# Optimization experiments

Measured on AMD Instinct MI355X. Metric: run time of the kernel, lower is better.

The kernel has to match this reference:

```python
import jax, jax.numpy as jnp
import numpy as np

B, L, D = 4, 2048, 1024
N_HEADS = 16
D_KV = D // N_HEADS  # 64
TEMPERATURE = D_KV ** 0.5  # 8.0 (note: applied even though heads are never split)


def setup_inputs() -> dict:
    key = jax.random.key(0)
    ks = jax.random.split(key, 7)
    s = 1.0 / np.sqrt(D)
    return {
        "Q": jax.random.normal(ks[0], (B, L, D), jnp.float32),
        "K": jax.random.normal(ks[1], (B, L, D), jnp.float32),
        "V": jax.random.normal(ks[2], (B, L, D), jnp.float32),
        # nn.Linear weights, shape [out, in]; y = x @ W.T
        "W_Q": jax.random.normal(ks[3], (D, D), jnp.float32) * s,
        "W_K": jax.random.normal(ks[4], (D, D), jnp.float32) * s,
        "W_V": jax.random.normal(ks[5], (D, D), jnp.float32) * s,
        "W_O": jax.random.normal(ks[6], (D, D), jnp.float32) * s,
        "masked": 0,
    }


def reference(Q, K, V, W_Q, W_K, W_V, W_O, masked):
    # projections (no bias)
    q = jnp.einsum("bld,ed->ble", Q, W_Q)
    k = jnp.einsum("bld,ed->ble", K, W_K)
    v = jnp.einsum("bld,ed->ble", V, W_V)
    # NOTE: original module never splits heads; scores contract over full d_model
    scores = jnp.einsum("bqe,bke->bqk", q, k) / TEMPERATURE  # [B, L, L]
    if masked:
        # faithful (buggy) original: fill where tril is True
        tril = jnp.tril(jnp.ones((L, L), dtype=bool))
        scores = jnp.where(tril[None], -jnp.inf, scores)
    attn_weights = jax.nn.softmax(scores, axis=-1)
    # dropout(0.1) disabled (eval mode)
    x = jnp.einsum("bqk,bke->bqe", attn_weights, v)
    out = jnp.einsum("ble,de->bld", x, W_O)
    return (out, attn_weights)
```

## Files before the change

kernel.cpp:

```cpp
#include <hip/hip_runtime.h>
#include <math.h>


static constexpr int B_ = 4;
static constexpr int L_ = 2048;
static constexpr int D_ = 1024;

#define BM 128
#define BN 128
#define BKK 64

typedef _Float16 f16x8 __attribute__((ext_vector_type(8)));
typedef float    f32x4 __attribute__((ext_vector_type(4)));
typedef short    s16x8 __attribute__((ext_vector_type(8)));
typedef unsigned short u16x4 __attribute__((ext_vector_type(4)));

typedef __attribute__((address_space(1))) const unsigned int GU32;
typedef __attribute__((address_space(3))) unsigned int LU32;

__device__ __forceinline__ void gload_lds16(const void* g, void* l) {
    __builtin_amdgcn_global_load_lds((GU32*)g, (LU32*)l, 16, 0, 0);
}

__device__ __forceinline__ short f2h_bits(float x) {
    union { _Float16 h; short s; } u;
    u.h = (_Float16)x;
    return u.s;
}

__device__ __forceinline__ s16x8 cvt8h(float4 a, float4 b) {
    union { _Float16 h[8]; s16x8 s; } u;
    u.h[0] = (_Float16)a.x; u.h[1] = (_Float16)a.y;
    u.h[2] = (_Float16)a.z; u.h[3] = (_Float16)a.w;
    u.h[4] = (_Float16)b.x; u.h[5] = (_Float16)b.y;
    u.h[6] = (_Float16)b.z; u.h[7] = (_Float16)b.w;
    return u.s;
}

__device__ __forceinline__ void compute_step(
    const short* __restrict__ As, const short* __restrict__ Bs,
    int wr, int wc, int lr, int lk, f32x4 (&acc)[4][4])
{
#pragma unroll
    for (int kk = 0; kk < 2; ++kk) {
        const int slotk = kk * 4 + lk;
        f16x8 a[4], b[4];
#pragma unroll
        for (int m = 0; m < 4; ++m) {
            const int r = wr * 64 + m * 16 + lr;
            a[m] = *(const f16x8*)&As[r * 64 + ((slotk ^ (r & 7)) << 3)];
        }
#pragma unroll
        for (int n = 0; n < 4; ++n) {
            const int c = wc * 64 + n * 16 + lr;
            b[n] = *(const f16x8*)&Bs[c * 64 + ((slotk ^ (c & 7)) << 3)];
        }
#pragma unroll
        for (int m = 0; m < 4; ++m)
#pragma unroll
            for (int n = 0; n < 4; ++n)
                acc[m][n] = __builtin_amdgcn_mfma_f32_16x16x32_f16(a[m], b[n], acc[m][n], 0, 0, 0);
    }
}

__global__ __launch_bounds__(256) void proj_qkv(
    const short* __restrict__ qf, const short* __restrict__ kf, const short* __restrict__ vf,
    const short* __restrict__ wq, const short* __restrict__ wk, const short* __restrict__ wv,
    short* __restrict__ qh, short* __restrict__ kh, short* __restrict__ vT)
{
    __shared__ short As[BM * BKK];
    __shared__ short Bs[BN * BKK];

    const int t    = threadIdx.x;
    const int wid  = t >> 6;
    const int lane = t & 63;
    const int bz   = blockIdx.z;

    const short* A16 = (bz == 0) ? qf : (bz == 1) ? kf : vf;
    const short* Bt  = (bz == 0) ? wq : (bz == 1) ? wk : wv;

    const int gx = gridDim.x, gy = gridDim.y;
    const int wg = blockIdx.y * gx + blockIdx.x;
    const int bm = (wg % gy) * BM;
    const int bn = (wg / gy) * BN;

    const int wr = wid >> 1, wc = wid & 1;
    const int lr = lane & 15, lk = lane >> 4;
    const int srow = t >> 3, sslot = t & 7;
    const int K = D_;

    f32x4 acc[4][4];
#pragma unroll
    for (int m = 0; m < 4; ++m)
#pragma unroll
        for (int n = 0; n < 4; ++n) acc[m][n] = (f32x4)0.f;

    for (int k0 = 0; k0 < K; k0 += BKK) {
        __syncthreads();
#pragma unroll
        for (int i = 0; i < 4; ++i) {
            const int rb = i * 32 + srow;
            const short* g = Bt + (long)(bn + rb) * K + k0 + ((sslot ^ (rb & 7)) << 3);
            gload_lds16(g, &Bs[i * 2048 + wid * 512]);
        }
#pragma unroll
        for (int i = 0; i < 4; ++i) {
            const int ra = i * 32 + srow;
            const short* g = A16 + (long)(bm + ra) * K + k0 + ((sslot ^ (ra & 7)) << 3);
            gload_lds16(g, &As[i * 2048 + wid * 512]);
        }
        __syncthreads();
        compute_step(As, Bs, wr, wc, lr, lk, acc);
    }

    const int N = D_;
    if (bz < 2) {
        short* C = (bz == 0) ? qh : kh;
#pragma unroll
        for (int m = 0; m < 4; ++m) {
            const int r0 = bm + wr * 64 + m * 16 + lk * 4;
#pragma unroll
            for (int n = 0; n < 4; ++n) {
                const int c = bn + wc * 64 + n * 16 + lr;
#pragma unroll
                for (int g = 0; g < 4; ++g)
                    C[(long)(r0 + g) * N + c] = f2h_bits(acc[m][n][g]);
            }
        }
    } else {
#pragma unroll
        for (int m = 0; m < 4; ++m) {
            const int rg = bm + wr * 64 + m * 16 + lk * 4;
            const long rb = (long)(rg >> 11) * ((long)N * L_) + (rg & (L_ - 1));
#pragma unroll
            for (int n = 0; n < 4; ++n) {
                const int c = bn + wc * 64 + n * 16 + lr;
                u16x4 v;
#pragma unroll
                for (int g = 0; g < 4; ++g) v[g] = (unsigned short)f2h_bits(acc[m][n][g]);
                *(u16x4*)&vT[rb + (long)c * L_] = v;
            }
        }
    }
}

template<int OMODE>
__global__ __launch_bounds__(256) void hgemm(
    const short* __restrict__ A16p, const short* __restrict__ Btp, void* __restrict__ Cp_,
    int M, int N, int K, long sA, long sB, long sC,
    float scale, int useMask, const int* __restrict__ mflag)
{
    __shared__ short As[BM * BKK];
    __shared__ short Bs[BN * BKK];

    const int t    = threadIdx.x;
    const int wid  = t >> 6;
    const int lane = t & 63;
    const int bz   = blockIdx.z;

    const int gx = gridDim.x, gy = gridDim.y;
    const int wg = blockIdx.y * gx + blockIdx.x;
    const int bm = (wg % gy) * BM;
    const int bn = (wg / gy) * BN;

    const short* Bt  = Btp + (long)bz * sB;
    const short* A16 = A16p + (long)bz * sA;

    const int wr = wid >> 1, wc = wid & 1;
    const int lr = lane & 15, lk = lane >> 4;
    const int srow = t >> 3, sslot = t & 7;

    f32x4 acc[4][4];
#pragma unroll
    for (int m = 0; m < 4; ++m)
#pragma unroll
        for (int n = 0; n < 4; ++n) acc[m][n] = (f32x4)0.f;

    for (int k0 = 0; k0 < K; k0 += BKK) {
        __syncthreads();
#pragma unroll
        for (int i = 0; i < 4; ++i) {
            const int rb = i * 32 + srow;
            const short* g = Bt + (long)(bn + rb) * K + k0 + ((sslot ^ (rb & 7)) << 3);
            gload_lds16(g, &Bs[i * 2048 + wid * 512]);
        }
#pragma unroll
        for (int i = 0; i < 4; ++i) {
            const int ra = i * 32 + srow;
            const short* g = A16 + (long)(bm + ra) * K + k0 + ((sslot ^ (ra & 7)) << 3);
            gload_lds16(g, &As[i * 2048 + wid * 512]);
        }
        __syncthreads();
        compute_step(As, Bs, wr, wc, lr, lk, acc);
    }

    if constexpr (OMODE == 2) {
        float* C = (float*)Cp_ + (long)bz * sC;
        const bool msk = useMask && (mflag[0] != 0);
#pragma unroll
        for (int m = 0; m < 4; ++m) {
            const int r0 = bm + wr * 64 + m * 16 + lk * 4;
#pragma unroll
            for (int n = 0; n < 4; ++n) {
                const int c = bn + wc * 64 + n * 16 + lr;
#pragma unroll
                for (int g = 0; g < 4; ++g) {
                    float v = acc[m][n][g] * scale;
                    if (msk && c <= r0 + g) v = -INFINITY;
                    C[(long)(r0 + g) * N + c] = v;
                }
            }
        }
    } else {
        short* C = (short*)Cp_ + (long)bz * sC;
#pragma unroll
        for (int m = 0; m < 4; ++m) {
            const int r0 = bm + wr * 64 + m * 16 + lk * 4;
#pragma unroll
            for (int n = 0; n < 4; ++n) {
                const int c = bn + wc * 64 + n * 16 + lr;
#pragma unroll
                for (int g = 0; g < 4; ++g)
                    C[(long)(r0 + g) * N + c] = f2h_bits(acc[m][n][g]);
            }
        }
    }
}

__global__ __launch_bounds__(256) void cvt_w4_k(
    const float* __restrict__ W_Q, const float* __restrict__ W_K,
    const float* __restrict__ W_V, const float* __restrict__ W_O,
    short* __restrict__ dst)
{
    const int w = blockIdx.y;
    const float* src = (w == 0) ? W_Q : (w == 1) ? W_K : (w == 2) ? W_V : W_O;
    short* out = dst + (size_t)w * D_ * D_;
    const int i = blockIdx.x * 256 + threadIdx.x;
    float4 a = ((const float4*)src)[2 * i];
    float4 b = ((const float4*)src)[2 * i + 1];
    *(s16x8*)&out[i * 8] = cvt8h(a, b);
}

__global__ __launch_bounds__(256) void cvt_qkv_k(
    const float* __restrict__ Q, const float* __restrict__ K,
    const float* __restrict__ V, short* __restrict__ dst)
{
    const int w = blockIdx.y;
    const float* src = (w == 0) ? Q : (w == 1) ? K : V;
    short* out = dst + (size_t)w * B_ * L_ * D_;
    const int i = blockIdx.x * 256 + threadIdx.x;
    float4 a = ((const float4*)src)[2 * i];
    float4 b = ((const float4*)src)[2 * i + 1];
    *(s16x8*)&out[i * 8] = cvt8h(a, b);
}

__global__ __launch_bounds__(256) void softmax_rows_k(
    float* __restrict__ S, short* __restrict__ S16)
{
    const long row = blockIdx.x;
    float* p = S + row * (long)L_;
    short* p16 = S16 + row * (long)L_;
    const int tid = threadIdx.x;

    float4 v0 = ((const float4*)p)[tid];
    float4 v1 = ((const float4*)p)[tid + 256];

    float m = fmaxf(fmaxf(fmaxf(v0.x, v0.y), fmaxf(v0.z, v0.w)),
                    fmaxf(fmaxf(v1.x, v1.y), fmaxf(v1.z, v1.w)));
#pragma unroll
    for (int o = 32; o > 0; o >>= 1) m = fmaxf(m, __shfl_xor(m, o, 64));

    __shared__ float wmax[4], wsum[4];
    if ((tid & 63) == 0) wmax[tid >> 6] = m;
    __syncthreads();
    m = fmaxf(fmaxf(wmax[0], wmax[1]), fmaxf(wmax[2], wmax[3]));

    v0.x = expf(v0.x - m); v0.y = expf(v0.y - m);
    v0.z = expf(v0.z - m); v0.w = expf(v0.w - m);
    v1.x = expf(v1.x - m); v1.y = expf(v1.y - m);
    v1.z = expf(v1.z - m); v1.w = expf(v1.w - m);

    float s = v0.x + v0.y + v0.z + v0.w + v1.x + v1.y + v1.z + v1.w;
#pragma unroll
    for (int o = 32; o > 0; o >>= 1) s += __shfl_xor(s, o, 64);
    if ((tid & 63) == 0) wsum[tid >> 6] = s;
    __syncthreads();
    s = wsum[0] + wsum[1] + wsum[2] + wsum[3];

    const float inv = 1.f / s;
    v0.x *= inv; v0.y *= inv; v0.z *= inv; v0.w *= inv;
    v1.x *= inv; v1.y *= inv; v1.z *= inv; v1.w *= inv;
    ((float4*)p)[tid] = v0;
    ((float4*)p)[tid + 256] = v1;

    union { _Float16 h[4]; u16x4 u; } h0, h1;
    h0.h[0] = (_Float16)v0.x; h0.h[1] = (_Float16)v0.y;
    h0.h[2] = (_Float16)v0.z; h0.h[3] = (_Float16)v0.w;
    h1.h[0] = (_Float16)v1.x; h1.h[1] = (_Float16)v1.y;
    h1.h[2] = (_Float16)v1.z; h1.h[3] = (_Float16)v1.w;
    ((u16x4*)p16)[tid] = h0.u;
    ((u16x4*)p16)[tid + 256] = h1.u;
}

extern "C" void kernel_launch(void* const* d_in, const int* in_sizes, int n_in,
                              void* d_out, int out_size, void* d_ws, size_t ws_size,
                              hipStream_t stream) {
    const float* Q   = (const float*)d_in[0];
    const float* K   = (const float*)d_in[1];
    const float* V   = (const float*)d_in[2];
    const float* W_Q = (const float*)d_in[3];
    const float* W_K = (const float*)d_in[4];
    const float* W_V = (const float*)d_in[5];
    const float* W_O = (const float*)d_in[6];
    const int* masked = (const int*)d_in[7];

    float* out  = (float*)d_out;
    float* attn = out + (size_t)B_ * L_ * D_;

    short* wq = (short*)d_ws;
    short* wk = wq + (size_t)D_ * D_;
    short* wv = wk + (size_t)D_ * D_;
    short* wo = wv + (size_t)D_ * D_;
    short* qh = wo + (size_t)D_ * D_;
    short* kh = qh + (size_t)B_ * L_ * D_;
    short* vT = kh + (size_t)B_ * L_ * D_;
    short* attn16 = vT + (size_t)B_ * L_ * D_;
    short* xh = qh;

    short* qf = (short*)attn;
    short* kf = qf + (size_t)B_ * L_ * D_;
    short* vf = kf + (size_t)B_ * L_ * D_;

    const long SLD = (long)L_ * D_;
    const long SLL = (long)L_ * L_;

    cvt_w4_k<<<dim3(D_ * D_ / 8 / 256, 4), 256, 0, stream>>>(W_Q, W_K, W_V, W_O, wq);
    cvt_qkv_k<<<dim3(B_ * L_ * D_ / 8 / 256, 3), 256, 0, stream>>>(Q, K, V, qf);

    proj_qkv<<<dim3(D_ / BN, (B_ * L_) / BM, 3), 256, 0, stream>>>(
        qf, kf, vf, wq, wk, wv, qh, kh, vT);

    dim3 gsc(L_ / BN, L_ / BM, B_);
    hgemm<2><<<gsc, 256, 0, stream>>>(qh, kh, attn, L_, L_, D_, SLD, SLD, SLL,
                                      0.125f, 1, masked);

    softmax_rows_k<<<dim3(B_ * L_), 256, 0, stream>>>(attn, attn16);

    dim3 gav(D_ / BN, L_ / BM, B_);
    hgemm<0><<<gav, 256, 0, stream>>>(attn16, vT, xh, L_, D_, L_, SLL, SLD, SLD,
                                      1.f, 0, masked);

    dim3 gproj(D_ / BN, (B_ * L_) / BM, 1);
    hgemm<2><<<gproj, 256, 0, stream>>>(xh, wo, out, B_ * L_, D_, D_, 0, 0, 0,
                                        1.f, 0, masked);
}
```

Before: 258.6 us.

## Store scores as fp16 and stage fp16 GEMM epilogues through LDS

The QK^T GEMM now writes scaled, masked scores in fp16 to the attn16 buffer instead of fp32 into the output. Softmax reads those fp16 scores and writes both the fp32 attention weights and the fp16 copy, which cuts the global write and read of the fp32 score matrix. The fp16 epilogues of the projection and GEMM kernels are also bounced through swizzled shared memory so each thread stores 16-byte coalesced rows instead of scattered 2-byte values. Rounding scores to fp16 before softmax adds error to the attention weights.

```diff
diff --git a/kernel.cpp b/kernel.cpp
--- a/kernel.cpp
+++ b/kernel.cpp
@@ -63,13 +63,49 @@
     }
 }
 
+template<int APPLY_SM>
+__device__ __forceinline__ void epilogue_f16_bounce(
+    short* __restrict__ lw, short* __restrict__ C, long N,
+    int bm, int bn, int wr, int wc, int lr, int lk, int lane,
+    const f32x4 (&acc)[4][4], float scale, bool msk)
+{
+#pragma unroll
+    for (int m = 0; m < 4; ++m) {
+        const int rl0 = m * 16 + lk * 4;
+#pragma unroll
+        for (int n = 0; n < 4; ++n) {
+            const int cl = n * 16 + lr;
+            const int slot = cl >> 3, cw = cl & 7;
+#pragma unroll
+            for (int g = 0; g < 4; ++g) {
+                const int rl = rl0 + g;
+                float v = acc[m][n][g];
+                if constexpr (APPLY_SM) {
+                    v *= scale;
+                    if (msk && (bn + wc * 64 + cl) <= (bm + wr * 64 + rl)) v = -INFINITY;
+                }
+                lw[rl * 64 + ((slot ^ (rl & 7)) << 3) + cw] = f2h_bits(v);
+            }
+        }
+    }
+    const int l8 = lane & 7, lr8 = lane >> 3;
+#pragma unroll
+    for (int it = 0; it < 8; ++it) {
+        const int rl = it * 8 + lr8;
+        const int cl = (l8 ^ (rl & 7)) << 3;
+        s16x8 d = *(const s16x8*)&lw[rl * 64 + (l8 << 3)];
+        *(s16x8*)&C[(long)(bm + wr * 64 + rl) * N + bn + wc * 64 + cl] = d;
+    }
+}
+
 __global__ __launch_bounds__(256) void proj_qkv(
     const short* __restrict__ qf, const short* __restrict__ kf, const short* __restrict__ vf,
     const short* __restrict__ wq, const short* __restrict__ wk, const short* __restrict__ wv,
     short* __restrict__ qh, short* __restrict__ kh, short* __restrict__ vT)
 {
-    __shared__ short As[BM * BKK];
-    __shared__ short Bs[BN * BKK];
+    __shared__ short smem[2 * BM * BKK];
+    short* As = smem;
+    short* Bs = smem + BM * BKK;
 
     const int t    = threadIdx.x;
     const int wid  = t >> 6;
@@ -115,18 +151,10 @@
 
     const int N = D_;
     if (bz < 2) {
+        __syncthreads();
         short* C = (bz == 0) ? qh : kh;
-#pragma unroll
-        for (int m = 0; m < 4; ++m) {
-            const int r0 = bm + wr * 64 + m * 16 + lk * 4;
-#pragma unroll
-            for (int n = 0; n < 4; ++n) {
-                const int c = bn + wc * 64 + n * 16 + lr;
-#pragma unroll
-                for (int g = 0; g < 4; ++g)
-                    C[(long)(r0 + g) * N + c] = f2h_bits(acc[m][n][g]);
-            }
-        }
+        epilogue_f16_bounce<0>(smem + wid * 4096, C, N, bm, bn, wr, wc, lr, lk, lane,
+                               acc, 1.f, false);
     } else {
 #pragma unroll
         for (int m = 0; m < 4; ++m) {
@@ -150,8 +178,9 @@
     int M, int N, int K, long sA, long sB, long sC,
     float scale, int useMask, const int* __restrict__ mflag)
 {
-    __shared__ short As[BM * BKK];
-    __shared__ short Bs[BN * BKK];
+    __shared__ short smem[2 * BM * BKK];
+    short* As = smem;
+    short* Bs = smem + BM * BKK;
 
     const int t    = threadIdx.x;
     const int wid  = t >> 6;
@@ -196,7 +225,6 @@
 
     if constexpr (OMODE == 2) {
         float* C = (float*)Cp_ + (long)bz * sC;
-        const bool msk = useMask && (mflag[0] != 0);
 #pragma unroll
         for (int m = 0; m < 4; ++m) {
             const int r0 = bm + wr * 64 + m * 16 + lk * 4;
@@ -204,26 +232,16 @@
             for (int n = 0; n < 4; ++n) {
                 const int c = bn + wc * 64 + n * 16 + lr;
 #pragma unroll
-                for (int g = 0; g < 4; ++g) {
-                    float v = acc[m][n][g] * scale;
-                    if (msk && c <= r0 + g) v = -INFINITY;
-                    C[(long)(r0 + g) * N + c] = v;
-                }
+                for (int g = 0; g < 4; ++g)
+                    C[(long)(r0 + g) * N + c] = acc[m][n][g] * scale;
             }
         }
     } else {
+        __syncthreads();
         short* C = (short*)Cp_ + (long)bz * sC;
-#pragma unroll
-        for (int m = 0; m < 4; ++m) {
-            const int r0 = bm + wr * 64 + m * 16 + lk * 4;
-#pragma unroll
-            for (int n = 0; n < 4; ++n) {
-                const int c = bn + wc * 64 + n * 16 + lr;
-#pragma unroll
-                for (int g = 0; g < 4; ++g)
-                    C[(long)(r0 + g) * N + c] = f2h_bits(acc[m][n][g]);
-            }
-        }
+        const bool msk = (OMODE == 3) && useMask && (mflag[0] != 0);
+        epilogue_f16_bounce<(OMODE == 3) ? 1 : 0>(
+            smem + wid * 4096, C, N, bm, bn, wr, wc, lr, lk, lane, acc, scale, msk);
     }
 }
 
@@ -255,18 +273,22 @@
 }
 
 __global__ __launch_bounds__(256) void softmax_rows_k(
-    float* __restrict__ S, short* __restrict__ S16)
+    short* __restrict__ S16, float* __restrict__ Sout)
 {
     const long row = blockIdx.x;
-    float* p = S + row * (long)L_;
     short* p16 = S16 + row * (long)L_;
+    float* pf  = Sout + row * (long)L_;
     const int tid = threadIdx.x;
 
-    float4 v0 = ((const float4*)p)[tid];
-    float4 v1 = ((const float4*)p)[tid + 256];
-
-    float m = fmaxf(fmaxf(fmaxf(v0.x, v0.y), fmaxf(v0.z, v0.w)),
-                    fmaxf(fmaxf(v1.x, v1.y), fmaxf(v1.z, v1.w)));
+    union { s16x8 v; _Float16 h[8]; } u;
+    u.v = ((const s16x8*)p16)[tid];
+    float f[8];
+#pragma unroll
+    for (int j = 0; j < 8; ++j) f[j] = (float)u.h[j];
+
+    float m = f[0];
+#pragma unroll
+    for (int j = 1; j < 8; ++j) m = fmaxf(m, f[j]);
 #pragma unroll
     for (int o = 32; o > 0; o >>= 1) m = fmaxf(m, __shfl_xor(m, o, 64));
 
@@ -275,12 +297,9 @@
     __syncthreads();
     m = fmaxf(fmaxf(wmax[0], wmax[1]), fmaxf(wmax[2], wmax[3]));
 
-    v0.x = expf(v0.x - m); v0.y = expf(v0.y - m);
-    v0.z = expf(v0.z - m); v0.w = expf(v0.w - m);
-    v1.x = expf(v1.x - m); v1.y = expf(v1.y - m);
-    v1.z = expf(v1.z - m); v1.w = expf(v1.w - m);
-
-    float s = v0.x + v0.y + v0.z + v0.w + v1.x + v1.y + v1.z + v1.w;
+    float s = 0.f;
+#pragma unroll
+    for (int j = 0; j < 8; ++j) { f[j] = expf(f[j] - m); s += f[j]; }
 #pragma unroll
     for (int o = 32; o > 0; o >>= 1) s += __shfl_xor(s, o, 64);
     if ((tid & 63) == 0) wsum[tid >> 6] = s;
@@ -288,18 +307,15 @@
     s = wsum[0] + wsum[1] + wsum[2] + wsum[3];
 
     const float inv = 1.f / s;
-    v0.x *= inv; v0.y *= inv; v0.z *= inv; v0.w *= inv;
-    v1.x *= inv; v1.y *= inv; v1.z *= inv; v1.w *= inv;
-    ((float4*)p)[tid] = v0;
-    ((float4*)p)[tid + 256] = v1;
-
-    union { _Float16 h[4]; u16x4 u; } h0, h1;
-    h0.h[0] = (_Float16)v0.x; h0.h[1] = (_Float16)v0.y;
-    h0.h[2] = (_Float16)v0.z; h0.h[3] = (_Float16)v0.w;
-    h1.h[0] = (_Float16)v1.x; h1.h[1] = (_Float16)v1.y;
-    h1.h[2] = (_Float16)v1.z; h1.h[3] = (_Float16)v1.w;
-    ((u16x4*)p16)[tid] = h0.u;
-    ((u16x4*)p16)[tid + 256] = h1.u;
+#pragma unroll
+    for (int j = 0; j < 8; ++j) f[j] = f[j] * inv;
+
+    float4 a, b;
+    a.x = f[0]; a.y = f[1]; a.z = f[2]; a.w = f[3];
+    b.x = f[4]; b.y = f[5]; b.z = f[6]; b.w = f[7];
+    ((float4*)pf)[2 * tid]     = a;
+    ((float4*)pf)[2 * tid + 1] = b;
+    ((s16x8*)p16)[tid] = cvt8h(a, b);
 }
 
 extern "C" void kernel_launch(void* const* d_in, const int* in_sizes, int n_in,
@@ -341,10 +357,10 @@
         qf, kf, vf, wq, wk, wv, qh, kh, vT);
 
     dim3 gsc(L_ / BN, L_ / BM, B_);
-    hgemm<2><<<gsc, 256, 0, stream>>>(qh, kh, attn, L_, L_, D_, SLD, SLD, SLL,
+    hgemm<3><<<gsc, 256, 0, stream>>>(qh, kh, attn16, L_, L_, D_, SLD, SLD, SLL,
                                       0.125f, 1, masked);
 
-    softmax_rows_k<<<dim3(B_ * L_), 256, 0, stream>>>(attn, attn16);
+    softmax_rows_k<<<dim3(B_ * L_), 256, 0, stream>>>(attn16, attn);
 
     dim3 gav(D_ / BN, L_ / BM, B_);
     hgemm<0><<<gav, 256, 0, stream>>>(attn16, vT, xh, L_, D_, L_, SLL, SLD, SLD,
```

After: 254.6 us. No clear change (-1.5%).
